# Kernel tuning notes

Measured on AMD Instinct MI355X. Metric: run time of the kernel, lower is better.

## Reference

```python
import jax, jax.numpy as jnp
import numpy as np

N, L, C = 4, 2048, 512
H, D = 8, 64          # head_num, head_channels; H*D == C so proj_in/out are Identity
FF = 4 * C            # GEGLU inner channels = 2048
EPS = 1e-5


def _layernorm(x, g, b):
    m = jnp.mean(x, axis=-1, keepdims=True)
    v = jnp.var(x, axis=-1, keepdims=True)
    return (x - m) * jax.lax.rsqrt(v + EPS) * g + b


def setup_inputs() -> dict:
    key = jax.random.key(0)
    ks = jax.random.split(key, 8)
    s = 0.02
    return {
        "x": jax.random.normal(ks[0], (N, L, C), dtype=jnp.float32),
        "ln0_g": jnp.ones((C,), jnp.float32),
        "ln0_b": jnp.zeros((C,), jnp.float32),
        "Wq": jax.random.normal(ks[1], (C, H * D), jnp.float32) * s,
        "bq": jnp.zeros((H * D,), jnp.float32),
        "Wk": jax.random.normal(ks[2], (C, H * D), jnp.float32) * s,
        "bk": jnp.zeros((H * D,), jnp.float32),
        "Wv": jax.random.normal(ks[3], (C, H * D), jnp.float32) * s,
        "bv": jnp.zeros((H * D,), jnp.float32),
        "ln1_g": jnp.ones((C,), jnp.float32),
        "ln1_b": jnp.zeros((C,), jnp.float32),
        "Wp": jax.random.normal(ks[4], (C, 2 * FF), jnp.float32) * s,
        "bp": jnp.zeros((2 * FF,), jnp.float32),
        "W2": jax.random.normal(ks[5], (FF, C), jnp.float32) * s,
        "b2": jnp.zeros((C,), jnp.float32),
    }


def reference(x, ln0_g, ln0_b, Wq, bq, Wk, bk, Wv, bv, ln1_g, ln1_b, Wp, bp, W2, b2):
    n, l, _ = x.shape
    # ---- self attention (CrossAttn with context = x) ----
    h = _layernorm(x, ln0_g, ln0_b)
    q = (h @ Wq + bq).reshape(n, l, H, D).transpose(0, 2, 1, 3)  # [n,H,l,D]
    k = (h @ Wk + bk).reshape(n, l, H, D).transpose(0, 2, 1, 3)
    v = (h @ Wv + bv).reshape(n, l, H, D).transpose(0, 2, 1, 3)
    scores = jnp.einsum('nhld,nhmd->nhlm', q, k) * (D ** -0.5)   # [n,H,l,l]
    attn = jax.nn.softmax(scores, axis=-1)
    o = jnp.einsum('nhlm,nhmd->nhld', attn, v)
    o = o.transpose(0, 2, 1, 3).reshape(n, l, H * D)
    # inner_channels == in_channels -> output projection is Identity (dropout=0)
    x = x + o
    # ---- feed forward: LayerNorm -> GEGLU -> Linear, residual ----
    h2 = _layernorm(x, ln1_g, ln1_b)
    pg = h2 @ Wp + bp                      # [n,l,2*FF]
    u, g = jnp.split(pg, 2, axis=-1)
    y = u * jax.nn.gelu(g, approximate=False)  # torch F.gelu default is exact erf
    return x + (y @ W2 + b2)
```

## Files before the change

kernel.cpp:

```cpp
#include <hip/hip_runtime.h>

typedef __attribute__((ext_vector_type(8))) short short8;
typedef __attribute__((ext_vector_type(4))) float f32x4;
typedef __attribute__((ext_vector_type(4))) unsigned short us4;

#define L_SEQ 2048
#define C_DIM 512
#define H_N 8
#define D_H 64
#define FF_DIM 2048

typedef __attribute__((address_space(3))) unsigned int as3_uint;
typedef const __attribute__((address_space(1))) unsigned int as1_uint;

__device__ __forceinline__ void gl16(const unsigned short* g, unsigned short* l) {
  __builtin_amdgcn_global_load_lds((as1_uint*)g, (as3_uint*)l, 16, 0, 0);
}

__device__ __forceinline__ unsigned short f2bf(float f) {
  unsigned int u = __float_as_uint(f);
  u = u + 0x7fffu + ((u >> 16) & 1u);
  return (unsigned short)(u >> 16);
}

__device__ __forceinline__ unsigned int cvtpk_bf16(float a, float b) {
  unsigned int r;
  asm("v_cvt_pk_bf16_f32 %0, %1, %2" : "=v"(r) : "v"(a), "v"(b));
  return r;
}

__global__ __launch_bounds__(256) void transpose_conv(
    const float* __restrict__ in, unsigned short* __restrict__ out,
    int R, int Ccols, int geglu) {
  __shared__ float tile[32][33];
  int tx = threadIdx.x & 31, ty = threadIdx.x >> 5;
  int c0 = blockIdx.x * 32, r0 = blockIdx.y * 32;
#pragma unroll
  for (int j = 0; j < 4; ++j) {
    int r = ty + j * 8;
    tile[r][tx] = in[(size_t)(r0 + r) * Ccols + c0 + tx];
  }
  __syncthreads();
#pragma unroll
  for (int j = 0; j < 4; ++j) {
    int rr = ty + j * 8;
    int n = c0 + rr;
    int J = n;
    if (geglu) {
      int hc = Ccols >> 1;
      J = (n < hc) ? (((n >> 4) << 5) + (n & 15))
                   : ((((n - hc) >> 4) << 5) + 16 + ((n - hc) & 15));
    }
    out[(size_t)J * R + r0 + tx] = f2bf(tile[tx][rr]);
  }
}

__global__ __launch_bounds__(256) void ln_kernel(
    const float* __restrict__ in, const float* __restrict__ g,
    const float* __restrict__ b, unsigned short* __restrict__ out) {
  int w = threadIdx.x >> 6, lane = threadIdx.x & 63;
  int row = blockIdx.x * 4 + w;
  const float4* p = (const float4*)(in + (size_t)row * C_DIM);
  float4 v0 = p[lane * 2], v1 = p[lane * 2 + 1];
  float s = v0.x + v0.y + v0.z + v0.w + v1.x + v1.y + v1.z + v1.w;
  float q = v0.x * v0.x + v0.y * v0.y + v0.z * v0.z + v0.w * v0.w +
            v1.x * v1.x + v1.y * v1.y + v1.z * v1.z + v1.w * v1.w;
#pragma unroll
  for (int m = 1; m < 64; m <<= 1) {
    s += __shfl_xor(s, m);
    q += __shfl_xor(q, m);
  }
  float mean = s * (1.0f / 512.0f);
  float var = q * (1.0f / 512.0f) - mean * mean;
  float rstd = rsqrtf(var + 1e-5f);
  const float4* gp = (const float4*)g;
  const float4* bp = (const float4*)b;
  float4 g0 = gp[lane * 2], g1 = gp[lane * 2 + 1];
  float4 b0 = bp[lane * 2], b1 = bp[lane * 2 + 1];
  short8 o;
  o[0] = (short)f2bf((v0.x - mean) * rstd * g0.x + b0.x);
  o[1] = (short)f2bf((v0.y - mean) * rstd * g0.y + b0.y);
  o[2] = (short)f2bf((v0.z - mean) * rstd * g0.z + b0.z);
  o[3] = (short)f2bf((v0.w - mean) * rstd * g0.w + b0.w);
  o[4] = (short)f2bf((v1.x - mean) * rstd * g1.x + b1.x);
  o[5] = (short)f2bf((v1.y - mean) * rstd * g1.y + b1.y);
  o[6] = (short)f2bf((v1.z - mean) * rstd * g1.z + b1.z);
  o[7] = (short)f2bf((v1.w - mean) * rstd * g1.w + b1.w);
  *((short8*)(out + (size_t)row * C_DIM) + lane) = o;
}

template <int EPI>
__global__ __launch_bounds__(256, 2) void gemm_kernel(
    const unsigned short* __restrict__ A, const unsigned short* __restrict__ Bt,
    int M, int N, int K,
    const float* __restrict__ bias0, const float* __restrict__ bias1,
    const float* __restrict__ bias2, const float* __restrict__ resid,
    void* __restrict__ outp) {
  __shared__ unsigned short As[128 * 32];
  __shared__ unsigned short Bs[128 * 32];
  int tid = threadIdx.x;
  int lane = tid & 63, w = tid >> 6;
  int wr = w >> 1, wc = w & 1;
  int hi = lane >> 4, l15 = lane & 15;
  int m0 = blockIdx.y * 128, n0 = blockIdx.x * 128;

  f32x4 acc[4][4];
#pragma unroll
  for (int i = 0; i < 4; ++i)
#pragma unroll
    for (int j = 0; j < 4; ++j) acc[i][j] = (f32x4){0.f, 0.f, 0.f, 0.f};

  int srow = w * 16 + (lane >> 2);
  int scol = (lane & 3) * 8;
  const unsigned short* aG0 = A + (size_t)(m0 + srow) * K + scol;
  const unsigned short* aG1 = A + (size_t)(m0 + 64 + srow) * K + scol;
  const unsigned short* bG0 = Bt + (size_t)(n0 + srow) * K + scol;
  const unsigned short* bG1 = Bt + (size_t)(n0 + 64 + srow) * K + scol;
  unsigned short* aL0 = &As[w * 512];
  unsigned short* aL1 = &As[2048 + w * 512];
  unsigned short* bL0 = &Bs[w * 512];
  unsigned short* bL1 = &Bs[2048 + w * 512];

  for (int k0 = 0; k0 < K; k0 += 32) {
    __syncthreads();
    gl16(aG0 + k0, aL0);
    gl16(aG1 + k0, aL1);
    gl16(bG0 + k0, bL0);
    gl16(bG1 + k0, bL1);
    __syncthreads();
    short8 af[4], bf[4];
#pragma unroll
    for (int mi = 0; mi < 4; ++mi)
      af[mi] = *(const short8*)&As[(wr * 64 + mi * 16 + l15) * 32 + hi * 8];
#pragma unroll
    for (int ni = 0; ni < 4; ++ni)
      bf[ni] = *(const short8*)&Bs[(wc * 64 + ni * 16 + l15) * 32 + hi * 8];
#pragma unroll
    for (int mi = 0; mi < 4; ++mi)
#pragma unroll
      for (int ni = 0; ni < 4; ++ni)
        acc[mi][ni] = __builtin_amdgcn_mfma_f32_16x16x32_bf16(
            af[mi], bf[ni], acc[mi][ni], 0, 0, 0);
  }

  if (EPI == 0) {
    unsigned short* out = (unsigned short*)outp;
#pragma unroll
    for (int mi = 0; mi < 4; ++mi) {
#pragma unroll
      for (int ni = 0; ni < 4; ++ni) {
        int col = n0 + wc * 64 + ni * 16 + l15;
        int t = col >> 9, jj = col & 511;
        int h = jj >> 6, d = jj & 63;
        const float* bptr = (t == 0) ? bias0 : (t == 1 ? bias1 : bias2);
        float bv = bptr[jj];
        int rbase = m0 + wr * 64 + mi * 16 + hi * 4;
        if (t == 2) {
          us4 pk;
#pragma unroll
          for (int i = 0; i < 4; ++i) pk[i] = f2bf(acc[mi][ni][i] + bv);
          int n = rbase >> 11, l = rbase & 2047;
          size_t dst = 8388608u + ((size_t)((n * H_N + h) * D_H + d)) * L_SEQ + l;
          *(us4*)(out + dst) = pk;
        } else {
#pragma unroll
          for (int i = 0; i < 4; ++i) {
            int m = rbase + i;
            int n = m >> 11, l = m & 2047;
            float val = acc[mi][ni][i] + bv;
            if (t == 0) val *= 0.18033688011112042f;
            size_t dst = (size_t)t * 4194304u +
                         (((size_t)(n * H_N + h)) * L_SEQ + l) * D_H + d;
            out[dst] = f2bf(val);
          }
        }
      }
    }
  } else if (EPI == 1) {
    unsigned short* out = (unsigned short*)outp;
#pragma unroll
    for (int mi = 0; mi < 4; ++mi) {
#pragma unroll
      for (int np = 0; np < 2; ++np) {
        int J16 = (n0 >> 4) + wc * 4 + np * 2;
        int ucol = (J16 >> 1) * 16 + l15;
        float bu = bias0[ucol], bg = bias0[2048 + ucol];
        int rbase = m0 + wr * 64 + mi * 16 + hi * 4;
#pragma unroll
        for (int i = 0; i < 4; ++i) {
          float uu = acc[mi][np * 2][i] + bu;
          float gg = acc[mi][np * 2 + 1][i] + bg;
          float ge = 0.5f * gg * (1.0f + erff(gg * 0.70710678118f));
          out[(size_t)(rbase + i) * FF_DIM + ucol] = f2bf(uu * ge);
        }
      }
    }
  } else {
    float* out = (float*)outp;
#pragma unroll
    for (int mi = 0; mi < 4; ++mi) {
#pragma unroll
      for (int ni = 0; ni < 4; ++ni) {
        int col = n0 + wc * 64 + ni * 16 + l15;
        float bv = bias0[col];
        int rbase = m0 + wr * 64 + mi * 16 + hi * 4;
#pragma unroll
        for (int i = 0; i < 4; ++i) {
          size_t idx = (size_t)(rbase + i) * C_DIM + col;
          out[idx] = acc[mi][ni][i] + bv + resid[idx];
        }
      }
    }
  }
}

__global__ __launch_bounds__(256, 3) void attn_kernel(
    const unsigned short* __restrict__ qkv, const float* __restrict__ x,
    float* __restrict__ x1) {
  __shared__ unsigned short Kb[2][4096];
  __shared__ unsigned short Vb[2][4096];
  __shared__ __align__(16) unsigned int Pl[4][16][36];

  int tid = threadIdx.x, lane = tid & 63, w = tid >> 6;
  int hi = lane >> 4, l15 = lane & 15;
  int bid = blockIdx.x;
  int k8 = bid & 7, j = bid >> 3;
  int nh = (k8 << 2) + (j & 3);
  int q0 = (j >> 2) << 6;
  int n = nh >> 3, h = nh & 7;
  const unsigned short* qb = qkv + (size_t)nh * (L_SEQ * D_H);
  const unsigned short* kb = qb + 4194304u;
  const unsigned short* vtb = qkv + 8388608u + (size_t)nh * (D_H * L_SEQ);

  short8 qf[2];
#pragma unroll
  for (int m = 0; m < 2; ++m)
    qf[m] = *(const short8*)(qb + (size_t)(q0 + w * 16 + l15) * D_H + m * 32 + hi * 8);

  f32x4 O[4];
#pragma unroll
  for (int c = 0; c < 4; ++c) O[c] = (f32x4){0.f, 0.f, 0.f, 0.f};
  float lsum = 0.f;

  int r8 = lane >> 3;
  int cb = ((lane & 7) ^ r8) * 8;

#define STAGE(tt, bb)                                                         \
  {                                                                           \
    int t0s = (tt) * 64;                                                      \
    _Pragma("unroll") for (int r2 = 0; r2 < 2; ++r2) {                        \
      int rowb = w * 16 + r2 * 8;                                             \
      gl16(kb + (size_t)(t0s + rowb + r8) * 64 + cb, &Kb[bb][rowb * 64]);     \
      gl16(vtb + (size_t)(rowb + r8) * 2048 + t0s + cb, &Vb[bb][rowb * 64]);  \
    }                                                                         \
  }

  STAGE(0, 0)
  int buf = 0;
  int swz = (l15 & 7) << 4;

  for (int t = 0; t < 32; ++t) {
    __syncthreads();
    if (t < 31) STAGE(t + 1, buf ^ 1)

    short8 kf[4][2];
#pragma unroll
    for (int mc = 0; mc < 4; ++mc)
#pragma unroll
      for (int m = 0; m < 2; ++m) {
        int off = (mc * 16 + l15) * 128 + ((m * 64 + hi * 16) ^ swz);
        kf[mc][m] = *(const short8*)((const char*)Kb[buf] + off);
      }

#pragma unroll
    for (int mc = 0; mc < 4; ++mc) {
      f32x4 s = (f32x4){0.f, 0.f, 0.f, 0.f};
      s = __builtin_amdgcn_mfma_f32_16x16x32_bf16(kf[mc][0], qf[0], s, 0, 0, 0);
      s = __builtin_amdgcn_mfma_f32_16x16x32_bf16(kf[mc][1], qf[1], s, 0, 0, 0);
      float p0 = __builtin_amdgcn_exp2f(s[0]);
      float p1 = __builtin_amdgcn_exp2f(s[1]);
      float p2 = __builtin_amdgcn_exp2f(s[2]);
      float p3 = __builtin_amdgcn_exp2f(s[3]);
      lsum += (p0 + p1) + (p2 + p3);
      uint2 pw;
      pw.x = cvtpk_bf16(p0, p1);
      pw.y = cvtpk_bf16(p2, p3);
      *(uint2*)&Pl[w][l15][mc * 8 + hi * 2] = pw;
    }

    short8 vf[4][2];
#pragma unroll
    for (int c = 0; c < 4; ++c)
#pragma unroll
      for (int m = 0; m < 2; ++m) {
        int off = (c * 16 + l15) * 128 + ((m * 64 + hi * 16) ^ swz);
        vf[c][m] = *(const short8*)((const char*)Vb[buf] + off);
      }
    short8 pf[2];
#pragma unroll
    for (int m = 0; m < 2; ++m)
      pf[m] = *(const short8*)&Pl[w][l15][m * 16 + hi * 4];
#pragma unroll
    for (int c = 0; c < 4; ++c) {
      O[c] = __builtin_amdgcn_mfma_f32_16x16x32_bf16(vf[c][0], pf[0], O[c], 0, 0, 0);
      O[c] = __builtin_amdgcn_mfma_f32_16x16x32_bf16(vf[c][1], pf[1], O[c], 0, 0, 0);
    }
    buf ^= 1;
  }

  lsum += __shfl_xor(lsum, 16);
  lsum += __shfl_xor(lsum, 32);
  float invl = 1.0f / lsum;

  int tok = q0 + w * 16 + l15;
  size_t base = ((size_t)(n * L_SEQ + tok)) * C_DIM + h * 64;
#pragma unroll
  for (int c = 0; c < 4; ++c) {
    const float4 xv = *(const float4*)(x + base + c * 16 + hi * 4);
    float4 ov;
    ov.x = xv.x + O[c][0] * invl;
    ov.y = xv.y + O[c][1] * invl;
    ov.z = xv.z + O[c][2] * invl;
    ov.w = xv.w + O[c][3] * invl;
    *(float4*)(x1 + base + c * 16 + hi * 4) = ov;
  }
#undef STAGE
}

extern "C" void kernel_launch(void* const* d_in, const int* in_sizes, int n_in,
                              void* d_out, int out_size, void* d_ws,
                              size_t ws_size, hipStream_t stream) {
  const float* x = (const float*)d_in[0];
  const float* ln0g = (const float*)d_in[1];
  const float* ln0b = (const float*)d_in[2];
  const float* Wq = (const float*)d_in[3];
  const float* bq = (const float*)d_in[4];
  const float* Wk = (const float*)d_in[5];
  const float* bk = (const float*)d_in[6];
  const float* Wv = (const float*)d_in[7];
  const float* bv = (const float*)d_in[8];
  const float* ln1g = (const float*)d_in[9];
  const float* ln1b = (const float*)d_in[10];
  const float* Wp = (const float*)d_in[11];
  const float* bp = (const float*)d_in[12];
  const float* W2 = (const float*)d_in[13];
  const float* b2 = (const float*)d_in[14];

  char* ws = (char*)d_ws;
  unsigned short* hbuf = (unsigned short*)ws;
  unsigned short* qkvb = (unsigned short*)(ws + 8388608);
  unsigned short* ybuf = (unsigned short*)ws;
  float* x1 = (float*)(ws + 33554432);
  unsigned short* h2 = (unsigned short*)(ws + 33554432 + 16777216);
  unsigned short* wqkvt = (unsigned short*)(ws + 33554432 + 16777216 + 8388608);
  unsigned short* wpt = wqkvt + 1536 * 512;
  unsigned short* w2t = wpt + 4096 * 512;

  transpose_conv<<<dim3(16, 16), 256, 0, stream>>>(Wq, wqkvt, 512, 512, 0);
  transpose_conv<<<dim3(16, 16), 256, 0, stream>>>(Wk, wqkvt + 262144, 512, 512, 0);
  transpose_conv<<<dim3(16, 16), 256, 0, stream>>>(Wv, wqkvt + 524288, 512, 512, 0);
  transpose_conv<<<dim3(128, 16), 256, 0, stream>>>(Wp, wpt, 512, 4096, 1);
  transpose_conv<<<dim3(16, 64), 256, 0, stream>>>(W2, w2t, 2048, 512, 0);

  ln_kernel<<<2048, 256, 0, stream>>>(x, ln0g, ln0b, hbuf);
  gemm_kernel<0><<<dim3(12, 64), 256, 0, stream>>>(hbuf, wqkvt, 8192, 1536, 512,
                                                   bq, bk, bv, nullptr, qkvb);
  attn_kernel<<<1024, 256, 0, stream>>>(qkvb, x, x1);
  ln_kernel<<<2048, 256, 0, stream>>>(x1, ln1g, ln1b, h2);
  gemm_kernel<1><<<dim3(32, 64), 256, 0, stream>>>(h2, wpt, 8192, 4096, 512, bp,
                                                   nullptr, nullptr, nullptr, ybuf);
  gemm_kernel<2><<<dim3(4, 64), 256, 0, stream>>>(ybuf, w2t, 8192, 512, 2048, b2,
                                                  nullptr, nullptr, x1,
                                                  (float*)d_out);
}
```

Measured before the change: 297.6 us.

## Split attention key sequence across two wave groups with LDS reduction

The attention kernel now launches 512 threads per block. Two halves of four waves each process separate halves of the key/value sequence using 32-token tiles, and their partial O accumulators and row sums are combined through LDS at the end. This doubles the waves available to hide latency and shortens each wave's serial loop. In exchange it adds a final reduction with extra barriers and uses smaller per-iteration tiles, which means more barriers per token processed.

```diff
diff --git a/kernel.cpp b/kernel.cpp
--- a/kernel.cpp
+++ b/kernel.cpp
@@ -214,14 +214,13 @@
   }
 }
 
-__global__ __launch_bounds__(256, 3) void attn_kernel(
+__global__ __launch_bounds__(512, 6) void attn_kernel(
     const unsigned short* __restrict__ qkv, const float* __restrict__ x,
     float* __restrict__ x1) {
-  __shared__ unsigned short Kb[2][4096];
-  __shared__ unsigned short Vb[2][4096];
-  __shared__ __align__(16) unsigned int Pl[4][16][36];
+  __shared__ __align__(16) char lds_raw[43008];
 
   int tid = threadIdx.x, lane = tid & 63, w = tid >> 6;
+  int half = w >> 2, wq = w & 3;
   int hi = lane >> 4, l15 = lane & 15;
   int bid = blockIdx.x;
   int k8 = bid & 7, j = bid >> 3;
@@ -235,24 +234,28 @@
   short8 qf[2];
 #pragma unroll
   for (int m = 0; m < 2; ++m)
-    qf[m] = *(const short8*)(qb + (size_t)(q0 + w * 16 + l15) * D_H + m * 32 + hi * 8);
+    qf[m] = *(const short8*)(qb + (size_t)(q0 + wq * 16 + l15) * D_H + m * 32 + hi * 8);
 
   f32x4 O[4];
 #pragma unroll
   for (int c = 0; c < 4; ++c) O[c] = (f32x4){0.f, 0.f, 0.f, 0.f};
   float lsum = 0.f;
 
-  int r8 = lane >> 3;
-  int cb = ((lane & 7) ^ r8) * 8;
-
-#define STAGE(tt, bb)                                                         \
-  {                                                                           \
-    int t0s = (tt) * 64;                                                      \
-    _Pragma("unroll") for (int r2 = 0; r2 < 2; ++r2) {                        \
-      int rowb = w * 16 + r2 * 8;                                             \
-      gl16(kb + (size_t)(t0s + rowb + r8) * 64 + cb, &Kb[bb][rowb * 64]);     \
-      gl16(vtb + (size_t)(rowb + r8) * 2048 + t0s + cb, &Vb[bb][rowb * 64]);  \
-    }                                                                         \
+  const int T0 = half << 10;
+  int kr = wq * 8 + (lane >> 3);
+  int kc = (((lane & 7) ^ (lane >> 3)) << 3);
+  int vr = wq * 16 + (lane >> 2);
+  int vc = (((lane & 3) ^ (vr & 3)) << 3);
+
+#define KBb(bb) ((unsigned short*)(lds_raw + (((half << 1) | (bb)) << 12)))
+#define VBb(bb) ((unsigned short*)(lds_raw + 16384 + (((half << 1) | (bb)) << 12)))
+  unsigned int* plw = (unsigned int*)(lds_raw + 32768 + w * 1280);
+
+#define STAGE(tt, bb)                                           \
+  {                                                             \
+    int t0s = T0 + (tt) * 32;                                   \
+    gl16(kb + (size_t)(t0s + kr) * 64 + kc, KBb(bb) + wq * 512);\
+    gl16(vtb + (size_t)vr * 2048 + t0s + vc, VBb(bb) + wq * 512);\
   }
 
   STAGE(0, 0)
@@ -263,17 +266,18 @@
     __syncthreads();
     if (t < 31) STAGE(t + 1, buf ^ 1)
 
-    short8 kf[4][2];
-#pragma unroll
-    for (int mc = 0; mc < 4; ++mc)
+    const char* Kbase = (const char*)KBb(buf);
+    short8 kf[2][2];
+#pragma unroll
+    for (int mc = 0; mc < 2; ++mc)
 #pragma unroll
       for (int m = 0; m < 2; ++m) {
         int off = (mc * 16 + l15) * 128 + ((m * 64 + hi * 16) ^ swz);
-        kf[mc][m] = *(const short8*)((const char*)Kb[buf] + off);
+        kf[mc][m] = *(const short8*)(Kbase + off);
       }
 
 #pragma unroll
-    for (int mc = 0; mc < 4; ++mc) {
+    for (int mc = 0; mc < 2; ++mc) {
       f32x4 s = (f32x4){0.f, 0.f, 0.f, 0.f};
       s = __builtin_amdgcn_mfma_f32_16x16x32_bf16(kf[mc][0], qf[0], s, 0, 0, 0);
       s = __builtin_amdgcn_mfma_f32_16x16x32_bf16(kf[mc][1], qf[1], s, 0, 0, 0);
@@ -285,46 +289,56 @@
       uint2 pw;
       pw.x = cvtpk_bf16(p0, p1);
       pw.y = cvtpk_bf16(p2, p3);
-      *(uint2*)&Pl[w][l15][mc * 8 + hi * 2] = pw;
-    }
-
-    short8 vf[4][2];
-#pragma unroll
-    for (int c = 0; c < 4; ++c)
-#pragma unroll
-      for (int m = 0; m < 2; ++m) {
-        int off = (c * 16 + l15) * 128 + ((m * 64 + hi * 16) ^ swz);
-        vf[c][m] = *(const short8*)((const char*)Vb[buf] + off);
-      }
-    short8 pf[2];
-#pragma unroll
-    for (int m = 0; m < 2; ++m)
-      pf[m] = *(const short8*)&Pl[w][l15][m * 16 + hi * 4];
+      *(uint2*)((char*)plw + (l15 * 20 + mc * 8 + hi * 2) * 4) = pw;
+    }
+
+    short8 pf = *(const short8*)((const char*)plw + l15 * 80 + hi * 16);
+    const char* Vbase = (const char*)VBb(buf);
 #pragma unroll
     for (int c = 0; c < 4; ++c) {
-      O[c] = __builtin_amdgcn_mfma_f32_16x16x32_bf16(vf[c][0], pf[0], O[c], 0, 0, 0);
-      O[c] = __builtin_amdgcn_mfma_f32_16x16x32_bf16(vf[c][1], pf[1], O[c], 0, 0, 0);
+      int off = (c * 16 + l15) * 64 + ((hi ^ (l15 & 3)) << 4);
+      short8 vf = *(const short8*)(Vbase + off);
+      O[c] = __builtin_amdgcn_mfma_f32_16x16x32_bf16(vf, pf, O[c], 0, 0, 0);
     }
     buf ^= 1;
   }
 
-  lsum += __shfl_xor(lsum, 16);
-  lsum += __shfl_xor(lsum, 32);
-  float invl = 1.0f / lsum;
-
-  int tok = q0 + w * 16 + l15;
-  size_t base = ((size_t)(n * L_SEQ + tok)) * C_DIM + h * 64;
-#pragma unroll
-  for (int c = 0; c < 4; ++c) {
-    const float4 xv = *(const float4*)(x + base + c * 16 + hi * 4);
-    float4 ov;
-    ov.x = xv.x + O[c][0] * invl;
-    ov.y = xv.y + O[c][1] * invl;
-    ov.z = xv.z + O[c][2] * invl;
-    ov.w = xv.w + O[c][3] * invl;
-    *(float4*)(x1 + base + c * 16 + hi * 4) = ov;
+  __syncthreads();
+  float* cm = (float*)lds_raw;
+  float* my = cm + (size_t)(wq * 64 + lane) * 20;
+  if (half == 1) {
+#pragma unroll
+    for (int c = 0; c < 4; ++c) *(f32x4*)(my + c * 4) = O[c];
+    my[16] = lsum;
+  }
+  __syncthreads();
+  if (half == 0) {
+#pragma unroll
+    for (int c = 0; c < 4; ++c) {
+      f32x4 ob = *(const f32x4*)(my + c * 4);
+      O[c][0] += ob[0]; O[c][1] += ob[1]; O[c][2] += ob[2]; O[c][3] += ob[3];
+    }
+    lsum += my[16];
+    lsum += __shfl_xor(lsum, 16);
+    lsum += __shfl_xor(lsum, 32);
+    float invl = 1.0f / lsum;
+
+    int tok = q0 + wq * 16 + l15;
+    size_t base = ((size_t)(n * L_SEQ + tok)) * C_DIM + h * 64;
+#pragma unroll
+    for (int c = 0; c < 4; ++c) {
+      const float4 xv = *(const float4*)(x + base + c * 16 + hi * 4);
+      float4 ov;
+      ov.x = xv.x + O[c][0] * invl;
+      ov.y = xv.y + O[c][1] * invl;
+      ov.z = xv.z + O[c][2] * invl;
+      ov.w = xv.w + O[c][3] * invl;
+      *(float4*)(x1 + base + c * 16 + hi * 4) = ov;
+    }
   }
 #undef STAGE
+#undef KBb
+#undef VBb
 }
 
 extern "C" void kernel_launch(void* const* d_in, const int* in_sizes, int n_in,
@@ -365,7 +379,7 @@
   ln_kernel<<<2048, 256, 0, stream>>>(x, ln0g, ln0b, hbuf);
   gemm_kernel<0><<<dim3(12, 64), 256, 0, stream>>>(hbuf, wqkvt, 8192, 1536, 512,
                                                    bq, bk, bv, nullptr, qkvb);
-  attn_kernel<<<1024, 256, 0, stream>>>(qkvb, x, x1);
+  attn_kernel<<<1024, 512, 0, stream>>>(qkvb, x, x1);
   ln_kernel<<<2048, 256, 0, stream>>>(x1, ln1g, ln1b, h2);
   gemm_kernel<1><<<dim3(32, 64), 256, 0, stream>>>(h2, wpt, 8192, 4096, 512, bp,
                                                    nullptr, nullptr, nullptr, ybuf);
```

Measured after the change: 280.4 us. -5.8%, faster.
